# Optimization experiments

Hardware: AMD Instinct MI355X
Metric: run time of the kernel (lower is better)

Reference implementation:

```python
import jax, jax.numpy as jnp
import numpy as np

D = 1024      # d_model
H = 16        # num_heads
HW = D // H   # head_width = 64
FF = 4 * D    # hidden_dim = 4096
BATCH = 2
T = 2048
EPS = 1e-5


def layer_norm(x, g, b):
    mu = jnp.mean(x, axis=-1, keepdims=True)
    var = jnp.mean(jnp.square(x - mu), axis=-1, keepdims=True)
    return (x - mu) * jax.lax.rsqrt(var + EPS) * g + b


def setup_inputs() -> dict:
    key = jax.random.key(0)
    ks = jax.random.split(key, 7)
    s = 0.02
    return {
        "x": jax.random.normal(ks[0], (BATCH, T, D), dtype=jnp.float32),
        "Wq": jax.random.normal(ks[1], (D, D), dtype=jnp.float32) * s,
        "Wk": jax.random.normal(ks[2], (D, D), dtype=jnp.float32) * s,
        "Wv": jax.random.normal(ks[3], (D, D), dtype=jnp.float32) * s,
        "W1": jax.random.normal(ks[4], (FF, D), dtype=jnp.float32) * s,
        "W2": jax.random.normal(ks[5], (D, FF), dtype=jnp.float32) * s,
        "g1": jnp.ones((D,), dtype=jnp.float32),
        "b1": jnp.zeros((D,), dtype=jnp.float32),
        "g2": jnp.ones((D,), dtype=jnp.float32),
        "b2": jnp.zeros((D,), dtype=jnp.float32),
    }


def reference(x, Wq, Wk, Wv, W1, W2, g1, b1, g2, b2):
    N, t, d = x.shape
    # norm1
    xn = layer_norm(x, g1, b1)

    # --- MHSA with ALiBi + causal mask (math mirrors torch module) ---
    def heads(y):  # (N,t,D) -> (N,H,t,HW)
        return y.reshape(N, t, H, HW).transpose(0, 2, 1, 3)

    q = heads(xn @ Wq.T)
    k = heads(xn @ Wk.T)
    v = heads(xn @ Wv.T)

    scores = jnp.einsum("nhqd,nhkd->nhqk", q, k) / np.sqrt(HW).astype(np.float32)

    pos = jnp.arange(t)
    rel = (pos[None, :] - pos[:, None]).astype(x.dtype)           # [t,t], rel[i,j]=j-i
    slopes = (2.0 ** (-(jnp.arange(1, H + 1)) * (8.0 / H))).astype(x.dtype)  # [H]
    alibi = slopes[:, None, None] * rel                            # [H,t,t]
    causal = jnp.where(pos[None, :] > pos[:, None],
                       jnp.array(-jnp.inf, x.dtype),
                       jnp.array(0.0, x.dtype))                    # [t,t]

    att = jax.nn.softmax(scores + alibi[None] + causal[None, None], axis=-1)
    o = jnp.einsum("nhqk,nhkd->nhqd", att, v)
    o = o.transpose(0, 2, 1, 3).reshape(N, t, d)

    att_out = xn + o

    # --- MLP: Linear -> SiLU -> Linear ---
    h = layer_norm(att_out, g2, b2)
    m = jax.nn.silu(h @ W1.T) @ W2.T
    return att_out + m
```

## Files before the change

kernel.cpp:

```cpp
#include <hip/hip_runtime.h>

#define DMODEL 1024
#define NHEAD  16
#define HWID   64
#define FFDIM  4096
#define NBATCH 2
#define SEQT   2048
#define NTOK   4096
#define QKLD   3072

using bf8    = __attribute__((ext_vector_type(8))) short;
using f32x4  = __attribute__((ext_vector_type(4))) float;
using f32x16 = __attribute__((ext_vector_type(16))) float;

__device__ inline short to_bf16(float f) {
  unsigned u = __float_as_uint(f);
  return (short)((u + 0x7fffu + ((u >> 16) & 1u)) >> 16);
}
__device__ inline float from_bf16(short s) {
  return __uint_as_float(((unsigned)(unsigned short)s) << 16);
}
__device__ inline float exp2_fast(float x) {
  float r;
  asm("v_exp_f32 %0, %1" : "=v"(r) : "v"(x));
  return r;
}
__device__ inline unsigned cvt_pk_bf16(float lo, float hi) {
  unsigned r;
  asm("v_cvt_pk_bf16_f32 %0, %1, %2" : "=v"(r) : "v"(lo), "v"(hi));
  return r;
}
__device__ inline void lds_load16(const void* g, void* l) {
  __builtin_amdgcn_global_load_lds(
      (const __attribute__((address_space(1))) void*)g,
      (__attribute__((address_space(3))) void*)l, 16, 0, 0);
}

__global__ __launch_bounds__(256)
void cvt_all(const float* __restrict__ Wq, const float* __restrict__ Wk,
             const float* __restrict__ Wv, const float* __restrict__ W1,
             const float* __restrict__ W2, short* __restrict__ wqkv,
             short* __restrict__ w1b, short* __restrict__ w2b) {
  int i = blockIdx.x * 256 + threadIdx.x;
  const float* src;
  short* dst;
  if (i < 1048576)      { src = W1; dst = w1b; }
  else if (i < 2097152) { src = W2; dst = w2b;            i -= 1048576; }
  else if (i < 2359296) { src = Wq; dst = wqkv;           i -= 2097152; }
  else if (i < 2621440) { src = Wk; dst = wqkv + 1048576; i -= 2359296; }
  else                  { src = Wv; dst = wqkv + 2097152; i -= 2621440; }
  float4 v = ((const float4*)src)[i];
  short4 o;
  o.x = to_bf16(v.x); o.y = to_bf16(v.y);
  o.z = to_bf16(v.z); o.w = to_bf16(v.w);
  ((short4*)dst)[i] = o;
}

__global__ __launch_bounds__(256)
void ln_kernel(const float* __restrict__ x, const float* __restrict__ g,
               const float* __restrict__ b, short* __restrict__ out) {
  const int row = blockIdx.x;
  const int t = threadIdx.x;
  const float4 v = ((const float4*)(x + (long)row * DMODEL))[t];
  float s  = v.x + v.y + v.z + v.w;
  float s2 = v.x * v.x + v.y * v.y + v.z * v.z + v.w * v.w;
#pragma unroll
  for (int m = 1; m < 64; m <<= 1) {
    s  += __shfl_xor(s, m);
    s2 += __shfl_xor(s2, m);
  }
  __shared__ float red[8];
  if ((t & 63) == 0) { red[t >> 6] = s; red[4 + (t >> 6)] = s2; }
  __syncthreads();
  s  = red[0] + red[1] + red[2] + red[3];
  s2 = red[4] + red[5] + red[6] + red[7];
  const float mu = s * (1.f / DMODEL);
  const float rs = rsqrtf(s2 * (1.f / DMODEL) - mu * mu + 1e-5f);
  const float4 gv = ((const float4*)g)[t];
  const float4 bv = ((const float4*)b)[t];
  short4 o;
  o.x = to_bf16((v.x - mu) * rs * gv.x + bv.x);
  o.y = to_bf16((v.y - mu) * rs * gv.y + bv.y);
  o.z = to_bf16((v.z - mu) * rs * gv.z + bv.z);
  o.w = to_bf16((v.w - mu) * rs * gv.w + bv.w);
  ((short4*)(out + (long)row * DMODEL))[t] = o;
}

template <int EPI>
__global__ __launch_bounds__(512, 2)
void gemm256(const short* __restrict__ A, const short* __restrict__ Bw,
             void* __restrict__ Cout, int N, int lda, int ldb, int Kslice,
             long zstride) {
  __shared__ short lds[2][2][16384];
  const int tid = threadIdx.x;
  const int wid = tid >> 6, lane = tid & 63;
  const int l15 = lane & 15, l4 = lane >> 4;
  const int wm = wid >> 2, wn = wid & 3;

  const int gx = gridDim.x, nwg = gx * gridDim.y;
  const int wg = blockIdx.y * gx + blockIdx.x;
  const int sw = (wg & 7) * (nwg >> 3) + (wg >> 3);
  const int sx = gx >> 2;
  const int st = sw >> 4, w16 = sw & 15;
  const long bm = (long)((st / sx) * 4 + (w16 >> 2)) * 256;
  const long bn = (long)((st % sx) * 4 + (w16 & 3)) * 256;
  const long kofs = (long)blockIdx.z * Kslice;
  const int NT = Kslice >> 6;

  long arow[2], brow[2];
  int  sgel[2], dofs[2];
#pragma unroll
  for (int l = 0; l < 2; ++l) {
    const int g = l * 512 + tid;
    const int row = g >> 2;
    sgel[l] = ((g & 3) ^ ((row >> 1) & 3)) * 8;
    dofs[l] = g * 16;
    arow[l] = (bm + row) * (long)lda + kofs;
    brow[l] = (bn + row) * (long)ldb + kofs;
  }
  auto stage_half = [&](int h) {
    if (h >= (NT << 2)) return;
    const int th = h >> 2, hi = h & 3, buf = th & 1;
    const int ks = hi >> 1, isA = hi & 1;
    char* db = (char*)&lds[buf][isA ? 0 : 1][0] + ks * 16384;
    const long kb = (long)th * 64 + ks * 32;
#pragma unroll
    for (int l = 0; l < 2; ++l) {
      const short* src = (isA ? A + arow[l] : Bw + brow[l]) + kb + sgel[l];
      lds_load16(src, db + dofs[l]);
    }
  };

  const int xsw = (l4 ^ ((l15 >> 1) & 3)) << 4;
  const int aofs = (wm * 128 + l15) * 64 + xsw;
  const int bofs = (wn * 64 + l15) * 64 + xsw;

  f32x4 acc[8][4] = {};
  bf8 fa[4], fa2[4], fb[4];

#define PH_MID                                             \
  __builtin_amdgcn_s_barrier();                            \
  __builtin_amdgcn_s_setprio(1);
#define PH_END                                             \
  __builtin_amdgcn_s_setprio(0);                           \
  __builtin_amdgcn_s_barrier();                            \
  asm volatile("" ::: "memory");

#pragma unroll
  for (int h = 0; h < 7; ++h) stage_half(h);
  asm volatile("s_waitcnt vmcnt(6)" ::: "memory");
  __builtin_amdgcn_s_barrier();
  asm volatile("" ::: "memory");

  for (int u = 0; u < NT; ++u) {
    const int buf = u & 1;
    const char* pa = (const char*)&lds[buf][0][0];
    const char* pb = (const char*)&lds[buf][1][0];
#pragma unroll
    for (int m = 0; m < 4; ++m) fa[m] = *(const bf8*)(pa + aofs + m * 1024);
#pragma unroll
    for (int n = 0; n < 4; ++n) fb[n] = *(const bf8*)(pb + bofs + n * 1024);
    stage_half(4 * u + 7);
    PH_MID
#pragma unroll
    for (int m = 0; m < 4; ++m)
#pragma unroll
      for (int n = 0; n < 4; ++n)
        acc[m][n] = __builtin_amdgcn_mfma_f32_16x16x32_bf16(fa[m], fb[n], acc[m][n], 0, 0, 0);
    PH_END
#pragma unroll
    for (int m = 0; m < 4; ++m) fa2[m] = *(const bf8*)(pa + aofs + (4 + m) * 1024);
    stage_half(4 * u + 8);
    PH_MID
#pragma unroll
    for (int m = 0; m < 4; ++m)
#pragma unroll
      for (int n = 0; n < 4; ++n)
        acc[4 + m][n] = __builtin_amdgcn_mfma_f32_16x16x32_bf16(fa2[m], fb[n], acc[4 + m][n], 0, 0, 0);
    PH_END
#pragma unroll
    for (int m = 0; m < 4; ++m) fa[m] = *(const bf8*)(pa + 16384 + aofs + m * 1024);
#pragma unroll
    for (int n = 0; n < 4; ++n) fb[n] = *(const bf8*)(pb + 16384 + bofs + n * 1024);
    stage_half(4 * u + 9);
    PH_MID
#pragma unroll
    for (int m = 0; m < 4; ++m)
#pragma unroll
      for (int n = 0; n < 4; ++n)
        acc[m][n] = __builtin_amdgcn_mfma_f32_16x16x32_bf16(fa[m], fb[n], acc[m][n], 0, 0, 0);
    PH_END
#pragma unroll
    for (int m = 0; m < 4; ++m) fa2[m] = *(const bf8*)(pa + 16384 + aofs + (4 + m) * 1024);
    stage_half(4 * u + 10);
    if (u <= NT - 3)      asm volatile("s_waitcnt vmcnt(6)" ::: "memory");
    else if (u == NT - 2) asm volatile("s_waitcnt vmcnt(0)" ::: "memory");
    PH_MID
#pragma unroll
    for (int m = 0; m < 4; ++m)
#pragma unroll
      for (int n = 0; n < 4; ++n)
        acc[4 + m][n] = __builtin_amdgcn_mfma_f32_16x16x32_bf16(fa2[m], fb[n], acc[4 + m][n], 0, 0, 0);
    PH_END
  }
#undef PH_MID
#undef PH_END

#pragma unroll
  for (int mg = 0; mg < 8; ++mg)
#pragma unroll
    for (int n = 0; n < 4; ++n) {
      const long col = bn + wn * 64 + n * 16 + l15;
#pragma unroll
      for (int r = 0; r < 4; ++r) {
        const long row = bm + wm * 128 + mg * 16 + l4 * 4 + r;
        float v = acc[mg][n][r];
        if (EPI == 0) {
          ((short*)Cout)[row * N + col] = to_bf16(v);
        } else if (EPI == 1) {
          ((short*)Cout)[row * N + col] = to_bf16(v / (1.f + __expf(-v)));
        } else {
          ((short*)Cout)[blockIdx.z * zstride + row * N + col] = to_bf16(v);
        }
      }
    }
}

__global__ __launch_bounds__(256)
void pack_kv(const short* __restrict__ qkv, short* __restrict__ Kp,
             short* __restrict__ Vp) {
  __shared__ short tile[64][72];
  const int bx = blockIdx.x, bh = blockIdx.y;
  const int b = bh >> 4, h = bh & 15;
  const int t = threadIdx.x;
  if (bx < 64) {
    const int g = bx;
    const int row = t >> 3, cc = t & 7, c = cc >> 1, hi = cc & 1;
    const bf8 v = *(const bf8*)&qkv[(long)(b * SEQT + g * 32 + row) * QKLD +
                                    1024 + h * HWID + c * 16 + hi * 8];
    *(bf8*)&Kp[(((long)bh * 256 + g * 4 + c) * 64 + hi * 32 + row) * 8] = v;
  } else {
    const int tc = bx - 64;
    {
      const int r = t >> 2, c = (t & 3) * 16;
      const long src = (long)(b * SEQT + tc * 64 + r) * QKLD + 2048 + h * HWID + c;
      *(bf8*)&tile[r][c]     = *(const bf8*)&qkv[src];
      *(bf8*)&tile[r][c + 8] = *(const bf8*)&qkv[src + 8];
    }
    __syncthreads();
    const int dg = t >> 7, ch = (t >> 5) & 3, row = t & 31;
#pragma unroll
    for (int hi = 0; hi < 2; ++hi) {
      short o[8];
#pragma unroll
      for (int j = 0; j < 8; ++j) o[j] = tile[ch * 16 + hi * 8 + j][dg * 32 + row];
      *(bf8*)&Vp[(((long)bh * 256 + dg * 128 + tc * 4 + ch) * 64 + hi * 32 + row) * 8] =
          *(bf8*)o;
    }
  }
}

__global__ __launch_bounds__(64, 2)
void attn_kernel(const short* __restrict__ qkv, const short* __restrict__ Kp,
                 const short* __restrict__ Vp, const short* __restrict__ xn,
                 float* __restrict__ att) {
  const int L = blockIdx.x;
  const int bh = (L & 7) * 4 + ((L >> 3) & 3);
  const int u = L >> 5;
  const int qtile = (u < 32) ? (63 - u) : (u - 32);
  const int b = bh >> 4, h = bh & 15;
  const int q0 = qtile * 32;
  const int lane = threadIdx.x;
  const int l31 = lane & 31, hi = lane >> 5;
  const long tokbase = (long)b * SEQT;

  bf8 qf[4];
  {
    const short* qrow = qkv + (tokbase + q0 + l31) * QKLD + h * HWID + hi * 8;
#pragma unroll
    for (int c = 0; c < 4; ++c) qf[c] = *(const bf8*)(qrow + c * 16);
  }

  const float slope2 = exp2f(-0.5f * (float)(h + 1)) * 1.44269504f;
  const float sc2 = 0.125f * 1.44269504f;
  float arr[16];
#pragma unroll
  for (int r = 0; r < 16; ++r) arr[r] = slope2 * (float)((r & 3) + 8 * (r >> 2));
  const float hofs = slope2 * 4.f * (float)hi;
  const float qabs = (float)(q0 + l31);

  float m2 = -1e30f, lsum = 0.f;
  f32x16 acc0 = {}, acc1 = {};
  const int ktm = q0 >> 6;
  const bf8* kfb = (const bf8*)Kp + (long)bh * 16384 + lane;
  const bf8* vfb = (const bf8*)Vp + (long)bh * 16384 + lane;

  bf8 kc[8], kn[8], vc[8];
#pragma unroll
  for (int c = 0; c < 4; ++c) {
    kc[c]     = kfb[c * 64];
    kc[4 + c] = kfb[256 + c * 64];
  }

#pragma unroll 2
  for (int kt = 0; kt <= ktm; ++kt) {
    const int k0 = kt * 64;
    const long vb = (long)kt * 256;
#pragma unroll
    for (int ch = 0; ch < 4; ++ch) {
      vc[ch]     = vfb[vb + ch * 64];
      vc[4 + ch] = vfb[8192 + vb + ch * 64];
    }
    const long nb = (long)(kt < ktm ? kt + 1 : kt) * 512;
#pragma unroll
    for (int c = 0; c < 4; ++c) {
      kn[c]     = kfb[nb + c * 64];
      kn[4 + c] = kfb[nb + 256 + c * 64];
    }
    f32x16 s0 = {}, s1 = {};
#pragma unroll
    for (int c = 0; c < 4; ++c) {
      s0 = __builtin_amdgcn_mfma_f32_32x32x16_bf16(kc[c], qf[c], s0, 0, 0, 0);
      s1 = __builtin_amdgcn_mfma_f32_32x32x16_bf16(kc[4 + c], qf[c], s1, 0, 0, 0);
    }
    const float base = slope2 * ((float)k0 - qabs) + hofs;
    float s[32];
#pragma unroll
    for (int r = 0; r < 16; ++r) {
      s[r]      = fmaf(s0[r], sc2, base + arr[r]);
      s[16 + r] = fmaf(s1[r], sc2, base + arr[r] + slope2 * 32.f);
    }
    if (kt == ktm) {
      const int qi = q0 + l31;
#pragma unroll
      for (int r = 0; r < 16; ++r) {
        const int krel = (r & 3) + 8 * (r >> 2) + 4 * hi;
        if (k0 + krel > qi)      s[r]      = -1e30f;
        if (k0 + 32 + krel > qi) s[16 + r] = -1e30f;
      }
    }
    float ma = s[0], mb = s[1], mc = s[2], md = s[3];
#pragma unroll
    for (int i = 4; i < 32; i += 4) {
      ma = fmaxf(ma, s[i]); mb = fmaxf(mb, s[i + 1]);
      mc = fmaxf(mc, s[i + 2]); md = fmaxf(md, s[i + 3]);
    }
    float pm = fmaxf(fmaxf(ma, mb), fmaxf(mc, md));
    pm = fmaxf(pm, __shfl_xor(pm, 32));
    if (!__all(pm - m2 <= 11.0f)) {
      const float nm = fmaxf(m2, pm);
      const float alpha = exp2_fast(m2 - nm);
      m2 = nm;
      lsum *= alpha;
      acc0 *= alpha;
      acc1 *= alpha;
    }
    float p[32];
#pragma unroll
    for (int i = 0; i < 32; ++i) p[i] = exp2_fast(s[i] - m2);
    float sa = p[0], sb = p[1], sc = p[2], sd = p[3];
#pragma unroll
    for (int i = 4; i < 32; i += 4) {
      sa += p[i]; sb += p[i + 1]; sc += p[i + 2]; sd += p[i + 3];
    }
    float rs = (sa + sb) + (sc + sd);
    rs += __shfl_xor(rs, 32);
    lsum += rs;
    unsigned cpk[16];
#pragma unroll
    for (int g = 0; g < 8; ++g) {
      cpk[g]     = cvt_pk_bf16(p[2 * g], p[2 * g + 1]);
      cpk[8 + g] = cvt_pk_bf16(p[16 + 2 * g], p[16 + 2 * g + 1]);
    }
    bf8 pb[4];
#pragma unroll
    for (int ch = 0; ch < 4; ++ch) {
      const int cb = (ch >> 1) * 8 + (ch & 1) * 4;
      unsigned u0 = cpk[cb + 0], u2 = cpk[cb + 2];
      unsigned u1 = cpk[cb + 1], u3 = cpk[cb + 3];
      asm("v_permlane32_swap_b32 %0, %1" : "+v"(u0), "+v"(u2));
      asm("v_permlane32_swap_b32 %0, %1" : "+v"(u1), "+v"(u3));
      union { unsigned u[4]; bf8 v; } f;
      f.u[0] = u0; f.u[1] = u1; f.u[2] = u2; f.u[3] = u3;
      pb[ch] = f.v;
    }
#pragma unroll
    for (int ch = 0; ch < 4; ++ch) {
      acc0 = __builtin_amdgcn_mfma_f32_32x32x16_bf16(vc[ch], pb[ch], acc0, 0, 0, 0);
      acc1 = __builtin_amdgcn_mfma_f32_32x32x16_bf16(vc[4 + ch], pb[ch], acc1, 0, 0, 0);
    }
#pragma unroll
    for (int i = 0; i < 8; ++i) kc[i] = kn[i];
  }

  __shared__ float Os[32 * 68];
  const float rl = 1.f / lsum;
#pragma unroll
  for (int r = 0; r < 16; ++r) {
    const int d0 = (r & 3) + 8 * (r >> 2) + 4 * hi;
    Os[l31 * 68 + d0]      = acc0[r] * rl;
    Os[l31 * 68 + 32 + d0] = acc1[r] * rl;
  }
  __syncthreads();
#pragma unroll
  for (int it = 0; it < 8; ++it) {
    const int idx = it * 64 + lane;
    const int row = idx >> 4, c4 = idx & 15;
    const float4 ov = *(const float4*)&Os[row * 68 + c4 * 4];
    const long gbase = (tokbase + q0 + row) * DMODEL + h * HWID + c4 * 4;
    const short4 xv = *(const short4*)&xn[gbase];
    float4 o;
    o.x = ov.x + from_bf16(xv.x);
    o.y = ov.y + from_bf16(xv.y);
    o.z = ov.z + from_bf16(xv.z);
    o.w = ov.w + from_bf16(xv.w);
    *(float4*)&att[gbase] = o;
  }
}

__global__ __launch_bounds__(256)
void combine_kernel(const short* __restrict__ p, float* __restrict__ dout, int n4) {
  int i = blockIdx.x * 256 + threadIdx.x;
  if (i < n4) {
    float4 a = ((const float4*)dout)[i];
    short4 b0 = ((const short4*)(p))[i];
    short4 b1 = ((const short4*)(p + 4194304))[i];
    short4 b2 = ((const short4*)(p + 8388608))[i];
    short4 b3 = ((const short4*)(p + 12582912))[i];
    a.x += (from_bf16(b0.x) + from_bf16(b1.x)) + (from_bf16(b2.x) + from_bf16(b3.x));
    a.y += (from_bf16(b0.y) + from_bf16(b1.y)) + (from_bf16(b2.y) + from_bf16(b3.y));
    a.z += (from_bf16(b0.z) + from_bf16(b1.z)) + (from_bf16(b2.z) + from_bf16(b3.z));
    a.w += (from_bf16(b0.w) + from_bf16(b1.w)) + (from_bf16(b2.w) + from_bf16(b3.w));
    ((float4*)dout)[i] = a;
  }
}

extern "C" void kernel_launch(void* const* d_in, const int* in_sizes, int n_in,
                              void* d_out, int out_size, void* d_ws, size_t ws_size,
                              hipStream_t stream) {
  (void)in_sizes; (void)n_in; (void)out_size; (void)ws_size;
  const float* x  = (const float*)d_in[0];
  const float* Wq = (const float*)d_in[1];
  const float* Wk = (const float*)d_in[2];
  const float* Wv = (const float*)d_in[3];
  const float* W1 = (const float*)d_in[4];
  const float* W2 = (const float*)d_in[5];
  const float* g1 = (const float*)d_in[6];
  const float* b1 = (const float*)d_in[7];
  const float* g2 = (const float*)d_in[8];
  const float* b2 = (const float*)d_in[9];

  char* ws = (char*)d_ws;
  const size_t MB = 1024 * 1024;
  short* wqkv_b = (short*)(ws + 0);
  short* w1_b   = (short*)(ws + 6  * MB);
  short* w2_b   = (short*)(ws + 14 * MB);
  short* xn     = (short*)(ws + 22 * MB);
  short* qkv    = (short*)(ws + 30 * MB);
  short* m1     = (short*)(ws + 22 * MB);
  short* Kp     = (short*)(ws + 54 * MB);
  short* Vp     = (short*)(ws + 62 * MB);
  short* hb     = (short*)(ws + 70 * MB);
  short* parts  = (short*)(ws + 54 * MB);
  float* att    = (float*)d_out;

  cvt_all<<<11264, 256, 0, stream>>>(Wq, Wk, Wv, W1, W2, wqkv_b, w1_b, w2_b);

  ln_kernel<<<NTOK, 256, 0, stream>>>(x, g1, b1, xn);

  gemm256<0><<<dim3(12, 16), 512, 0, stream>>>(xn, wqkv_b, qkv, QKLD, DMODEL, DMODEL,
                                               DMODEL, 0);
  pack_kv<<<dim3(96, 32), 256, 0, stream>>>(qkv, Kp, Vp);

  attn_kernel<<<2048, 64, 0, stream>>>(qkv, Kp, Vp, xn, att);

  ln_kernel<<<NTOK, 256, 0, stream>>>(att, g2, b2, hb);

  gemm256<1><<<dim3(16, 16), 512, 0, stream>>>(hb, w1_b, m1, FFDIM, DMODEL, DMODEL,
                                               DMODEL, 0);
  gemm256<2><<<dim3(4, 16, 4), 512, 0, stream>>>(m1, w2_b, parts, DMODEL, FFDIM, FFDIM,
                                                 1024, (long)NTOK * DMODEL);
  combine_kernel<<<4096, 256, 0, stream>>>(parts, (float*)d_out, 1048576);
}
```

Baseline: 197.9 us.

## Pre-pack weights in MFMA fragment order and load B directly to registers

The weight conversion kernel now writes bf16 weights in a per-lane MFMA fragment layout, so each GEMM wave can fetch its B operand straight from global memory into registers without going through LDS. The GEMM is restructured around 32-wide K tiles with a triple-buffered LDS ring for A only and double-buffered B registers, with one barrier per tile. The aim is to halve LDS traffic and footprint and simplify the pipeline. The cost is more global/L2 traffic for B, since each wave loads its own B fragments with no sharing across wm, and a shorter K step per barrier.

```diff
diff --git a/kernel.cpp b/kernel.cpp
--- a/kernel.cpp
+++ b/kernel.cpp
@@ -37,23 +37,42 @@
 }
 
 __global__ __launch_bounds__(256)
-void cvt_all(const float* __restrict__ Wq, const float* __restrict__ Wk,
-             const float* __restrict__ Wv, const float* __restrict__ W1,
-             const float* __restrict__ W2, short* __restrict__ wqkv,
-             short* __restrict__ w1b, short* __restrict__ w2b) {
-  int i = blockIdx.x * 256 + threadIdx.x;
-  const float* src;
-  short* dst;
-  if (i < 1048576)      { src = W1; dst = w1b; }
-  else if (i < 2097152) { src = W2; dst = w2b;            i -= 1048576; }
-  else if (i < 2359296) { src = Wq; dst = wqkv;           i -= 2097152; }
-  else if (i < 2621440) { src = Wk; dst = wqkv + 1048576; i -= 2359296; }
-  else                  { src = Wv; dst = wqkv + 2097152; i -= 2621440; }
-  float4 v = ((const float4*)src)[i];
-  short4 o;
-  o.x = to_bf16(v.x); o.y = to_bf16(v.y);
-  o.z = to_bf16(v.z); o.w = to_bf16(v.w);
-  ((short4*)dst)[i] = o;
+void cvt_pack(const float* __restrict__ Wq, const float* __restrict__ Wk,
+              const float* __restrict__ Wv, const float* __restrict__ W1,
+              const float* __restrict__ W2, short* __restrict__ qkvP,
+              short* __restrict__ w1P, short* __restrict__ w2P) {
+  const int j = blockIdx.x * 256 + threadIdx.x;
+  const float* p;
+  short* o;
+  if (j < 98304) {
+    const int l15 = j & 15, r = j >> 4;
+    const int ks = r & 31, nblk = r >> 5;
+    const int n = nblk * 16 + l15;
+    const float* W = (n < 1024) ? Wq : (n < 2048) ? Wk : Wv;
+    p = W + (long)(n & 1023) * 1024 + ks * 32;
+    o = qkvP + ((long)(nblk * 32 + ks) * 64 + l15) * 8;
+  } else if (j < 229376) {
+    const int j2 = j - 98304;
+    const int l15 = j2 & 15, r = j2 >> 4;
+    const int ks = r & 31, nblk = r >> 5;
+    p = W1 + (long)(nblk * 16 + l15) * 1024 + ks * 32;
+    o = w1P + ((long)(nblk * 32 + ks) * 64 + l15) * 8;
+  } else {
+    const int j3 = j - 229376;
+    const int l15 = j3 & 15, r = j3 >> 4;
+    const int ks = r & 127, nblk = r >> 7;
+    p = W2 + (long)(nblk * 16 + l15) * 4096 + ks * 32;
+    o = w2P + ((long)(nblk * 128 + ks) * 64 + l15) * 8;
+  }
+#pragma unroll
+  for (int l4 = 0; l4 < 4; ++l4) {
+    const float4 a = *(const float4*)(p + l4 * 8);
+    const float4 b = *(const float4*)(p + l4 * 8 + 4);
+    short t[8];
+    t[0] = to_bf16(a.x); t[1] = to_bf16(a.y); t[2] = to_bf16(a.z); t[3] = to_bf16(a.w);
+    t[4] = to_bf16(b.x); t[5] = to_bf16(b.y); t[6] = to_bf16(b.z); t[7] = to_bf16(b.w);
+    *(bf8*)(o + l4 * 128) = *(bf8*)t;
+  }
 }
 
 __global__ __launch_bounds__(256)
@@ -88,10 +107,10 @@
 
 template <int EPI>
 __global__ __launch_bounds__(512, 2)
-void gemm256(const short* __restrict__ A, const short* __restrict__ Bw,
-             void* __restrict__ Cout, int N, int lda, int ldb, int Kslice,
+void gemm_bg(const short* __restrict__ A, const short* __restrict__ Bp,
+             void* __restrict__ Cout, int N, int lda, int KS, int Kslice,
              long zstride) {
-  __shared__ short lds[2][2][16384];
+  __shared__ short lds[3][8192];
   const int tid = threadIdx.x;
   const int wid = tid >> 6, lane = tid & 63;
   const int l15 = lane & 15, l4 = lane >> 4;
@@ -104,107 +123,70 @@
   const int st = sw >> 4, w16 = sw & 15;
   const long bm = (long)((st / sx) * 4 + (w16 >> 2)) * 256;
   const long bn = (long)((st % sx) * 4 + (w16 & 3)) * 256;
-  const long kofs = (long)blockIdx.z * Kslice;
-  const int NT = Kslice >> 6;
-
-  long arow[2], brow[2];
-  int  sgel[2], dofs[2];
+  const int kofs = blockIdx.z * Kslice;
+  const int NT = Kslice >> 5;
+
+  long arow[2];
+  int  dofs[2];
 #pragma unroll
   for (int l = 0; l < 2; ++l) {
     const int g = l * 512 + tid;
     const int row = g >> 2;
-    sgel[l] = ((g & 3) ^ ((row >> 1) & 3)) * 8;
+    const int sg = ((g & 3) ^ ((row >> 1) & 3)) * 8;
+    arow[l] = (bm + row) * (long)lda + kofs + sg;
     dofs[l] = g * 16;
-    arow[l] = (bm + row) * (long)lda + kofs;
-    brow[l] = (bn + row) * (long)ldb + kofs;
-  }
-  auto stage_half = [&](int h) {
-    if (h >= (NT << 2)) return;
-    const int th = h >> 2, hi = h & 3, buf = th & 1;
-    const int ks = hi >> 1, isA = hi & 1;
-    char* db = (char*)&lds[buf][isA ? 0 : 1][0] + ks * 16384;
-    const long kb = (long)th * 64 + ks * 32;
-#pragma unroll
-    for (int l = 0; l < 2; ++l) {
-      const short* src = (isA ? A + arow[l] : Bw + brow[l]) + kb + sgel[l];
-      lds_load16(src, db + dofs[l]);
-    }
+  }
+  const bf8* bp = (const bf8*)Bp;
+  long bidx[4];
+#pragma unroll
+  for (int i = 0; i < 4; ++i)
+    bidx[i] = ((long)((bn >> 4) + wn * 4 + i)) * KS + (kofs >> 5);
+  const int xsw = (l4 ^ ((l15 >> 1) & 3)) << 4;
+  int aofs[8];
+#pragma unroll
+  for (int m = 0; m < 8; ++m)
+    aofs[m] = (wm * 128 + m * 16 + l15) * 64 + xsw;
+
+  f32x4 acc[8][4] = {};
+  bf8 b0[4], b1[4];
+
+  auto stageA = [&](int t) {
+    char* db = (char*)&lds[t % 3][0];
+#pragma unroll
+    for (int l = 0; l < 2; ++l)
+      lds_load16(A + arow[l] + (long)t * 32, db + dofs[l]);
   };
-
-  const int xsw = (l4 ^ ((l15 >> 1) & 3)) << 4;
-  const int aofs = (wm * 128 + l15) * 64 + xsw;
-  const int bofs = (wn * 64 + l15) * 64 + xsw;
-
-  f32x4 acc[8][4] = {};
-  bf8 fa[4], fa2[4], fb[4];
-
-#define PH_MID                                             \
-  __builtin_amdgcn_s_barrier();                            \
-  __builtin_amdgcn_s_setprio(1);
-#define PH_END                                             \
-  __builtin_amdgcn_s_setprio(0);                           \
-  __builtin_amdgcn_s_barrier();                            \
-  asm volatile("" ::: "memory");
-
-#pragma unroll
-  for (int h = 0; h < 7; ++h) stage_half(h);
-  asm volatile("s_waitcnt vmcnt(6)" ::: "memory");
-  __builtin_amdgcn_s_barrier();
-  asm volatile("" ::: "memory");
-
-  for (int u = 0; u < NT; ++u) {
-    const int buf = u & 1;
-    const char* pa = (const char*)&lds[buf][0][0];
-    const char* pb = (const char*)&lds[buf][1][0];
-#pragma unroll
-    for (int m = 0; m < 4; ++m) fa[m] = *(const bf8*)(pa + aofs + m * 1024);
-#pragma unroll
-    for (int n = 0; n < 4; ++n) fb[n] = *(const bf8*)(pb + bofs + n * 1024);
-    stage_half(4 * u + 7);
-    PH_MID
-#pragma unroll
-    for (int m = 0; m < 4; ++m)
+  auto loadB = [&](int t, bf8 (&dst)[4]) {
+#pragma unroll
+    for (int i = 0; i < 4; ++i)
+      dst[i] = bp[(bidx[i] + t) * 64 + lane];
+  };
+  auto tile = [&](int t, bf8 (&cur)[4], bf8 (&nxt)[4]) {
+    asm volatile("s_waitcnt vmcnt(6)" ::: "memory");
+    __builtin_amdgcn_s_barrier();
+    asm volatile("" ::: "memory");
+    stageA(t + 2 < NT ? t + 2 : NT - 1);
+    loadB(t + 1 < NT ? t + 1 : NT - 1, nxt);
+    const char* pa = (const char*)&lds[t % 3][0];
+    bf8 fa[8];
+#pragma unroll
+    for (int m = 0; m < 8; ++m) fa[m] = *(const bf8*)(pa + aofs[m]);
+    __builtin_amdgcn_s_setprio(1);
+#pragma unroll
+    for (int m = 0; m < 8; ++m)
 #pragma unroll
       for (int n = 0; n < 4; ++n)
-        acc[m][n] = __builtin_amdgcn_mfma_f32_16x16x32_bf16(fa[m], fb[n], acc[m][n], 0, 0, 0);
-    PH_END
-#pragma unroll
-    for (int m = 0; m < 4; ++m) fa2[m] = *(const bf8*)(pa + aofs + (4 + m) * 1024);
-    stage_half(4 * u + 8);
-    PH_MID
-#pragma unroll
-    for (int m = 0; m < 4; ++m)
-#pragma unroll
-      for (int n = 0; n < 4; ++n)
-        acc[4 + m][n] = __builtin_amdgcn_mfma_f32_16x16x32_bf16(fa2[m], fb[n], acc[4 + m][n], 0, 0, 0);
-    PH_END
-#pragma unroll
-    for (int m = 0; m < 4; ++m) fa[m] = *(const bf8*)(pa + 16384 + aofs + m * 1024);
-#pragma unroll
-    for (int n = 0; n < 4; ++n) fb[n] = *(const bf8*)(pb + 16384 + bofs + n * 1024);
-    stage_half(4 * u + 9);
-    PH_MID
-#pragma unroll
-    for (int m = 0; m < 4; ++m)
-#pragma unroll
-      for (int n = 0; n < 4; ++n)
-        acc[m][n] = __builtin_amdgcn_mfma_f32_16x16x32_bf16(fa[m], fb[n], acc[m][n], 0, 0, 0);
-    PH_END
-#pragma unroll
-    for (int m = 0; m < 4; ++m) fa2[m] = *(const bf8*)(pa + 16384 + aofs + (4 + m) * 1024);
-    stage_half(4 * u + 10);
-    if (u <= NT - 3)      asm volatile("s_waitcnt vmcnt(6)" ::: "memory");
-    else if (u == NT - 2) asm volatile("s_waitcnt vmcnt(0)" ::: "memory");
-    PH_MID
-#pragma unroll
-    for (int m = 0; m < 4; ++m)
-#pragma unroll
-      for (int n = 0; n < 4; ++n)
-        acc[4 + m][n] = __builtin_amdgcn_mfma_f32_16x16x32_bf16(fa2[m], fb[n], acc[4 + m][n], 0, 0, 0);
-    PH_END
-  }
-#undef PH_MID
-#undef PH_END
+        acc[m][n] = __builtin_amdgcn_mfma_f32_16x16x32_bf16(fa[m], cur[n], acc[m][n], 0, 0, 0);
+    __builtin_amdgcn_s_setprio(0);
+  };
+
+  stageA(0);
+  stageA(1);
+  loadB(0, b0);
+  for (int t = 0; t < NT; t += 2) {
+    tile(t, b0, b1);
+    tile(t + 1, b1, b0);
+  }
 
 #pragma unroll
   for (int mg = 0; mg < 8; ++mg)
@@ -452,23 +434,23 @@
 
   char* ws = (char*)d_ws;
   const size_t MB = 1024 * 1024;
-  short* wqkv_b = (short*)(ws + 0);
-  short* w1_b   = (short*)(ws + 6  * MB);
-  short* w2_b   = (short*)(ws + 14 * MB);
-  short* xn     = (short*)(ws + 22 * MB);
-  short* qkv    = (short*)(ws + 30 * MB);
-  short* m1     = (short*)(ws + 22 * MB);
-  short* Kp     = (short*)(ws + 54 * MB);
-  short* Vp     = (short*)(ws + 62 * MB);
-  short* hb     = (short*)(ws + 70 * MB);
-  short* parts  = (short*)(ws + 54 * MB);
-  float* att    = (float*)d_out;
-
-  cvt_all<<<11264, 256, 0, stream>>>(Wq, Wk, Wv, W1, W2, wqkv_b, w1_b, w2_b);
+  short* qkvP  = (short*)(ws + 0);
+  short* w1P   = (short*)(ws + 6  * MB);
+  short* w2P   = (short*)(ws + 14 * MB);
+  short* xn    = (short*)(ws + 22 * MB);
+  short* qkv   = (short*)(ws + 30 * MB);
+  short* m1    = (short*)(ws + 22 * MB);
+  short* Kp    = (short*)(ws + 54 * MB);
+  short* Vp    = (short*)(ws + 62 * MB);
+  short* hb    = (short*)(ws + 70 * MB);
+  short* parts = (short*)(ws + 54 * MB);
+  float* att   = (float*)d_out;
+
+  cvt_pack<<<1408, 256, 0, stream>>>(Wq, Wk, Wv, W1, W2, qkvP, w1P, w2P);
 
   ln_kernel<<<NTOK, 256, 0, stream>>>(x, g1, b1, xn);
 
-  gemm256<0><<<dim3(12, 16), 512, 0, stream>>>(xn, wqkv_b, qkv, QKLD, DMODEL, DMODEL,
+  gemm_bg<0><<<dim3(12, 16), 512, 0, stream>>>(xn, qkvP, qkv, QKLD, DMODEL, 32,
                                                DMODEL, 0);
   pack_kv<<<dim3(96, 32), 256, 0, stream>>>(qkv, Kp, Vp);
 
@@ -476,9 +458,9 @@
 
   ln_kernel<<<NTOK, 256, 0, stream>>>(att, g2, b2, hb);
 
-  gemm256<1><<<dim3(16, 16), 512, 0, stream>>>(hb, w1_b, m1, FFDIM, DMODEL, DMODEL,
+  gemm_bg<1><<<dim3(16, 16), 512, 0, stream>>>(hb, w1P, m1, FFDIM, DMODEL, 32,
                                                DMODEL, 0);
-  gemm256<2><<<dim3(4, 16, 4), 512, 0, stream>>>(m1, w2_b, parts, DMODEL, FFDIM, FFDIM,
+  gemm_bg<2><<<dim3(4, 16, 4), 512, 0, stream>>>(m1, w2P, parts, DMODEL, FFDIM, 128,
                                                  1024, (long)NTOK * DMODEL);
   combine_kernel<<<4096, 256, 0, stream>>>(parts, (float*)d_out, 1048576);
 }
```

After: 205.0 us. 3.6% more time.

## Fuse K/V packing into QKV GEMM epilogue and drop pack_kv kernel

Applied to the files above, without the earlier changes.

The QKV projection GEMM gets a new epilogue that scatters Q, K and V straight into the fragment-packed layouts the attention kernel reads, so the separate pack_kv kernel is removed. Q now also uses the packed layout, which gives per-lane contiguous loads in attention. This saves one launch and a full read and write of the QKV tensor. In exchange, the epilogue does scattered scalar 2-byte stores, which may coalesce poorly and slow the GEMM.

```diff
diff --git a/kernel.cpp b/kernel.cpp
--- a/kernel.cpp
+++ b/kernel.cpp
@@ -219,49 +219,34 @@
           ((short*)Cout)[row * N + col] = to_bf16(v);
         } else if (EPI == 1) {
           ((short*)Cout)[row * N + col] = to_bf16(v / (1.f + __expf(-v)));
+        } else if (EPI == 2) {
+          ((short*)Cout)[blockIdx.z * zstride + row * N + col] = to_bf16(v);
         } else {
-          ((short*)Cout)[blockIdx.z * zstride + row * N + col] = to_bf16(v);
+          const int t  = (int)row;
+          const int cc = (int)col;
+          const int sec = cc >> 10;
+          const int h = (cc >> 6) & 15, hw = cc & 63;
+          const int bh = (t >> 11) * 16 + h, tl = t & 2047;
+          short* dst = (short*)Cout + (long)sec * 4194304;
+          long fi;
+          int  s, e;
+          if (sec < 2) {
+            fi = (long)bh * 256 + (tl >> 5) * 4 + (hw >> 4);
+            s  = ((hw >> 3) & 1) * 32 + (tl & 31);
+            e  = hw & 7;
+          } else {
+            fi = (long)bh * 256 + (hw >> 5) * 128 + (tl >> 6) * 4 + ((tl >> 4) & 3);
+            s  = ((tl >> 3) & 1) * 32 + (hw & 31);
+            e  = tl & 7;
+          }
+          dst[(fi * 64 + s) * 8 + e] = to_bf16(v);
         }
       }
     }
 }
 
-__global__ __launch_bounds__(256)
-void pack_kv(const short* __restrict__ qkv, short* __restrict__ Kp,
-             short* __restrict__ Vp) {
-  __shared__ short tile[64][72];
-  const int bx = blockIdx.x, bh = blockIdx.y;
-  const int b = bh >> 4, h = bh & 15;
-  const int t = threadIdx.x;
-  if (bx < 64) {
-    const int g = bx;
-    const int row = t >> 3, cc = t & 7, c = cc >> 1, hi = cc & 1;
-    const bf8 v = *(const bf8*)&qkv[(long)(b * SEQT + g * 32 + row) * QKLD +
-                                    1024 + h * HWID + c * 16 + hi * 8];
-    *(bf8*)&Kp[(((long)bh * 256 + g * 4 + c) * 64 + hi * 32 + row) * 8] = v;
-  } else {
-    const int tc = bx - 64;
-    {
-      const int r = t >> 2, c = (t & 3) * 16;
-      const long src = (long)(b * SEQT + tc * 64 + r) * QKLD + 2048 + h * HWID + c;
-      *(bf8*)&tile[r][c]     = *(const bf8*)&qkv[src];
-      *(bf8*)&tile[r][c + 8] = *(const bf8*)&qkv[src + 8];
-    }
-    __syncthreads();
-    const int dg = t >> 7, ch = (t >> 5) & 3, row = t & 31;
-#pragma unroll
-    for (int hi = 0; hi < 2; ++hi) {
-      short o[8];
-#pragma unroll
-      for (int j = 0; j < 8; ++j) o[j] = tile[ch * 16 + hi * 8 + j][dg * 32 + row];
-      *(bf8*)&Vp[(((long)bh * 256 + dg * 128 + tc * 4 + ch) * 64 + hi * 32 + row) * 8] =
-          *(bf8*)o;
-    }
-  }
-}
-
 __global__ __launch_bounds__(64, 2)
-void attn_kernel(const short* __restrict__ qkv, const short* __restrict__ Kp,
+void attn_kernel(const short* __restrict__ Qp, const short* __restrict__ Kp,
                  const short* __restrict__ Vp, const short* __restrict__ xn,
                  float* __restrict__ att) {
   const int L = blockIdx.x;
@@ -276,9 +261,9 @@
 
   bf8 qf[4];
   {
-    const short* qrow = qkv + (tokbase + q0 + l31) * QKLD + h * HWID + hi * 8;
-#pragma unroll
-    for (int c = 0; c < 4; ++c) qf[c] = *(const bf8*)(qrow + c * 16);
+    const bf8* qfb = (const bf8*)Qp + (long)bh * 16384 + (long)qtile * 4 * 64 + lane;
+#pragma unroll
+    for (int c = 0; c < 4; ++c) qf[c] = qfb[c * 64];
   }
 
   const float slope2 = exp2f(-0.5f * (float)(h + 1)) * 1.44269504f;
@@ -456,11 +441,9 @@
   short* w1_b   = (short*)(ws + 6  * MB);
   short* w2_b   = (short*)(ws + 14 * MB);
   short* xn     = (short*)(ws + 22 * MB);
-  short* qkv    = (short*)(ws + 30 * MB);
+  short* QKVp   = (short*)(ws + 30 * MB);
+  short* hb     = (short*)(ws + 54 * MB);
   short* m1     = (short*)(ws + 22 * MB);
-  short* Kp     = (short*)(ws + 54 * MB);
-  short* Vp     = (short*)(ws + 62 * MB);
-  short* hb     = (short*)(ws + 70 * MB);
   short* parts  = (short*)(ws + 54 * MB);
   float* att    = (float*)d_out;
 
@@ -468,11 +451,10 @@
 
   ln_kernel<<<NTOK, 256, 0, stream>>>(x, g1, b1, xn);
 
-  gemm256<0><<<dim3(12, 16), 512, 0, stream>>>(xn, wqkv_b, qkv, QKLD, DMODEL, DMODEL,
+  gemm256<3><<<dim3(12, 16), 512, 0, stream>>>(xn, wqkv_b, QKVp, QKLD, DMODEL, DMODEL,
                                                DMODEL, 0);
-  pack_kv<<<dim3(96, 32), 256, 0, stream>>>(qkv, Kp, Vp);
-
-  attn_kernel<<<2048, 64, 0, stream>>>(qkv, Kp, Vp, xn, att);
+
+  attn_kernel<<<2048, 64, 0, stream>>>(QKVp, QKVp + 4194304, QKVp + 8388608, xn, att);
 
   ln_kernel<<<NTOK, 256, 0, stream>>>(att, g2, b2, hb);
 
```

Result: no change. 200.0 us (+1.1%).
